# Kernel tuning notes

Measured on AMD Instinct MI355X. Metric: run time of the kernel, lower is better.

The kernel has to match this reference:

```python
import jax, jax.numpy as jnp
import numpy as np

B, S, D, H = 4, 2048, 1024, 16
DK = D // H

def setup_inputs() -> dict:
    key = jax.random.key(0)
    ks = jax.random.split(key, 8)
    scale = 1.0 / np.sqrt(D)
    return {
        'q': jax.random.normal(ks[0], (B, S, D), jnp.float32),
        'k': jax.random.normal(ks[1], (B, S, D), jnp.float32),
        'v': jax.random.normal(ks[2], (B, S, D), jnp.float32),
        'Wq': jax.random.normal(ks[3], (D, D), jnp.float32) * scale,
        'bq': jnp.zeros((D,), jnp.float32),
        'Wk': jax.random.normal(ks[4], (D, D), jnp.float32) * scale,
        'bk': jnp.zeros((D,), jnp.float32),
        'Wv': jax.random.normal(ks[5], (D, D), jnp.float32) * scale,
        'bv': jnp.zeros((D,), jnp.float32),
        'Wo': jax.random.normal(ks[6], (D, D), jnp.float32) * scale,
        'bo': jnp.zeros((D,), jnp.float32),
    }

def reference(q, k, v, Wq, bq, Wk, bk, Wv, bv, Wo, bo):
    # Linear projections (torch Linear: x @ W.T + b; here W stored as [in,out])
    qp = q @ Wq + bq  # [B,S,D]
    kp = k @ Wk + bk
    vp = v @ Wv + bv
    # split heads -> [B,H,S,DK]
    qh = qp.reshape(B, S, H, DK).transpose(0, 2, 1, 3)
    kh = kp.reshape(B, S, H, DK).transpose(0, 2, 1, 3)
    vh = vp.reshape(B, S, H, DK).transpose(0, 2, 1, 3)
    scores = jnp.einsum('bhqd,bhkd->bhqk', qh, kh) / jnp.sqrt(jnp.float32(DK))
    attn = jax.nn.softmax(scores, axis=-1)  # [B,H,S,S]
    out = jnp.einsum('bhqk,bhkd->bhqd', attn, vh)
    out = out.transpose(0, 2, 1, 3).reshape(B, S, D)
    return out @ Wo + bo
```

## Files before the change

### kernel.cpp

```cpp
#include <hip/hip_runtime.h>
#include <math.h>

#define SEQ 2048
#define DIM 1024
#define NH 16

typedef short s8v __attribute__((ext_vector_type(8)));
typedef float f4v __attribute__((ext_vector_type(4)));

__device__ __forceinline__ unsigned short f2bf(float x) {
    unsigned u = __float_as_uint(x);
    u += 0x7FFFu + ((u >> 16) & 1u);
    return (unsigned short)(u >> 16);
}
__device__ __forceinline__ unsigned short f2bf_fast(float x) {
    return (unsigned short)((__float_as_uint(x) + 0x8000u) >> 16);
}

__global__ void conv3_f32_bf16(const float* __restrict__ q, const float* __restrict__ k,
                               const float* __restrict__ v,
                               unsigned short* __restrict__ qb, unsigned short* __restrict__ kb,
                               unsigned short* __restrict__ vb, int n4) {
    const float* in = (blockIdx.y == 0) ? q : (blockIdx.y == 1) ? k : v;
    unsigned short* out = (blockIdx.y == 0) ? qb : (blockIdx.y == 1) ? kb : vb;
    int i = blockIdx.x * 256 + threadIdx.x;
    if (i >= n4) return;
    float4 x = ((const float4*)in)[i];
    ushort4 o;
    o.x = f2bf(x.x); o.y = f2bf(x.y); o.z = f2bf(x.z); o.w = f2bf(x.w);
    ((ushort4*)out)[i] = o;
}

__global__ __launch_bounds__(256)
void convT4_f32_bf16(const float* __restrict__ W0, const float* __restrict__ W1,
                     const float* __restrict__ W2, const float* __restrict__ W3,
                     unsigned short* __restrict__ T0, unsigned short* __restrict__ T1,
                     unsigned short* __restrict__ T2, unsigned short* __restrict__ T3) {
    const float* W = (blockIdx.z == 0) ? W0 : (blockIdx.z == 1) ? W1 : (blockIdx.z == 2) ? W2 : W3;
    unsigned short* WT = (blockIdx.z == 0) ? T0 : (blockIdx.z == 1) ? T1 : (blockIdx.z == 2) ? T2 : T3;
    __shared__ float T[64][65];
    const int t = threadIdx.x;
    const int n0 = blockIdx.x * 64, k0 = blockIdx.y * 64;
    #pragma unroll
    for (int i = 0; i < 4; i++) {
        int idx = t + i * 256;
        int r = idx >> 4, c4 = idx & 15;
        float4 v = *(const float4*)&W[(size_t)(k0 + r) * DIM + n0 + c4 * 4];
        T[r][c4 * 4 + 0] = v.x; T[r][c4 * 4 + 1] = v.y;
        T[r][c4 * 4 + 2] = v.z; T[r][c4 * 4 + 3] = v.w;
    }
    __syncthreads();
    #pragma unroll
    for (int i = 0; i < 4; i++) {
        int idx = t + i * 256;
        int rn = idx >> 4, c4 = idx & 15;
        ushort4 o;
        o.x = f2bf(T[c4 * 4 + 0][rn]);
        o.y = f2bf(T[c4 * 4 + 1][rn]);
        o.z = f2bf(T[c4 * 4 + 2][rn]);
        o.w = f2bf(T[c4 * 4 + 3][rn]);
        *(ushort4*)&WT[(size_t)(n0 + rn) * DIM + k0 + c4 * 4] = o;
    }
}

template<int MODE>
__device__ __forceinline__
void gemm_core(const unsigned short* __restrict__ A,
               const unsigned short* __restrict__ BT,
               const float* __restrict__ bias, void* __restrict__ outp,
               float scale, int bx, int by)
{
    __shared__ __align__(16) unsigned short As[128 * 64];
    __shared__ __align__(16) unsigned short Bs[128 * 64];
    const int t = threadIdx.x;
    const int lane = t & 63, w = t >> 6;
    const int l15 = lane & 15, quad = lane >> 4;
    const int bm = by * 128, bn = bx * 128;
    const int wm = (w & 1) * 64, wn = (w >> 1) * 64;
    const int lrow = lane >> 3, lcol = (lane & 7) * 8;

    f4v acc[4][4];
    #pragma unroll
    for (int mi = 0; mi < 4; mi++)
        #pragma unroll
        for (int ni = 0; ni < 4; ni++)
            acc[mi][ni] = (f4v){0.f, 0.f, 0.f, 0.f};

    for (int k0 = 0; k0 < DIM; k0 += 64) {
        __syncthreads();
        #pragma unroll
        for (int i = 0; i < 4; i++) {
            int ci = w + i * 4;
            int row = ci * 8 + lrow;
            __builtin_amdgcn_global_load_lds(
                (const __attribute__((address_space(1))) unsigned int*)
                    (A + (size_t)(bm + row) * DIM + k0 + lcol),
                (__attribute__((address_space(3))) unsigned int*)(As + ci * 8 * 64),
                16, 0, 0);
            __builtin_amdgcn_global_load_lds(
                (const __attribute__((address_space(1))) unsigned int*)
                    (BT + (size_t)(bn + row) * DIM + k0 + lcol),
                (__attribute__((address_space(3))) unsigned int*)(Bs + ci * 8 * 64),
                16, 0, 0);
        }
        __syncthreads();
        #pragma unroll
        for (int kc = 0; kc < 2; kc++) {
            const int ko = kc * 32 + quad * 8;
            s8v af[4], bf[4];
            #pragma unroll
            for (int mi = 0; mi < 4; mi++)
                af[mi] = *(const s8v*)&As[(wm + mi * 16 + l15) * 64 + ko];
            #pragma unroll
            for (int ni = 0; ni < 4; ni++)
                bf[ni] = *(const s8v*)&Bs[(wn + ni * 16 + l15) * 64 + ko];
            #pragma unroll
            for (int mi = 0; mi < 4; mi++)
                #pragma unroll
                for (int ni = 0; ni < 4; ni++)
                    acc[mi][ni] = __builtin_amdgcn_mfma_f32_16x16x32_bf16(
                        af[mi], bf[ni], acc[mi][ni], 0, 0, 0);
        }
    }

    #pragma unroll
    for (int mi = 0; mi < 4; mi++) {
        #pragma unroll
        for (int ni = 0; ni < 4; ni++) {
            #pragma unroll
            for (int r = 0; r < 4; r++) {
                int m = bm + wm + mi * 16 + quad * 4 + r;
                int n = bn + wn + ni * 16 + l15;
                float val = acc[mi][ni][r] + bias[n];
                if (MODE == 0) {
                    ((float*)outp)[(size_t)m * DIM + n] = val;
                } else {
                    val *= scale;
                    int b = m >> 11, s = m & (SEQ - 1);
                    int h = n >> 6, dk = n & 63;
                    ((unsigned short*)outp)[(((size_t)(b * NH + h)) * SEQ + s) * 64 + dk] = f2bf(val);
                }
            }
        }
    }
}

__global__ __launch_bounds__(256)
void qkv_gemm(const unsigned short* __restrict__ qb, const unsigned short* __restrict__ kb,
              const unsigned short* __restrict__ vb,
              const unsigned short* __restrict__ WqT, const unsigned short* __restrict__ WkT,
              const unsigned short* __restrict__ WvT,
              const float* __restrict__ bq, const float* __restrict__ bk,
              const float* __restrict__ bv,
              unsigned short* __restrict__ qp, unsigned short* __restrict__ kp,
              unsigned short* __restrict__ vp)
{
    const int z = blockIdx.z;
    const unsigned short* A  = (z == 0) ? qb : (z == 1) ? kb : vb;
    const unsigned short* BT = (z == 0) ? WqT : (z == 1) ? WkT : WvT;
    const float* bias        = (z == 0) ? bq : (z == 1) ? bk : bv;
    unsigned short* outp     = (z == 0) ? qp : (z == 1) ? kp : vp;
    float scale = (z == 0) ? 0.125f : 1.0f;
    gemm_core<1>(A, BT, bias, outp, scale, blockIdx.x, blockIdx.y);
}

__global__ __launch_bounds__(256)
void out_gemm(const unsigned short* __restrict__ A, const unsigned short* __restrict__ BT,
              const float* __restrict__ bias, float* __restrict__ outp)
{
    gemm_core<0>(A, BT, bias, outp, 1.0f, blockIdx.x, blockIdx.y);
}

__global__ __launch_bounds__(256)
void transp_v(const unsigned short* __restrict__ vp, unsigned short* __restrict__ vpT) {
    __shared__ unsigned short T[64 * 72];
    const int t = threadIdx.x;
    const int bh = blockIdx.y, s0 = blockIdx.x * 64;
    const int r = t >> 3, c = (t & 7) * 8;
    #pragma unroll
    for (int i = 0; i < 2; i++) {
        int row = r + i * 32;
        *(s8v*)&T[row * 72 + c] = *(const s8v*)&vp[((size_t)bh * SEQ + s0 + row) * 64 + c];
    }
    __syncthreads();
    #pragma unroll
    for (int i = 0; i < 2; i++) {
        int d = r + i * 32;
        s8v o;
        #pragma unroll
        for (int j = 0; j < 8; j++) o[j] = (short)T[(c + j) * 72 + d];
        *(s8v*)&vpT[((size_t)bh * 64 + d) * SEQ + s0 + c] = o;
    }
}

__global__ __launch_bounds__(256)
void attn_mfma(const unsigned short* __restrict__ Q,
               const unsigned short* __restrict__ Kp,
               const unsigned short* __restrict__ VT,
               unsigned short* __restrict__ AO)
{
    __shared__ __align__(16) unsigned short Ks[64 * 72];
    __shared__ __align__(16) unsigned short Vs[64 * 72];
    __shared__ __align__(16) unsigned short Ps[4][32 * 72];
    const int t = threadIdx.x;
    const int lane = t & 63, w = t >> 6;
    const int l15 = lane & 15, quad = lane >> 4;
    const int bh = blockIdx.y, q0 = blockIdx.x * 128;

    const unsigned short* qbase = Q + ((size_t)bh * SEQ + q0 + w * 32) * 64;
    const unsigned short* kbase = Kp + (size_t)bh * SEQ * 64;
    const unsigned short* vtbase = VT + (size_t)bh * 64 * SEQ;

    s8v qf[2][2];
    #pragma unroll
    for (int qs = 0; qs < 2; qs++)
        #pragma unroll
        for (int kc = 0; kc < 2; kc++)
            qf[qs][kc] = *(const s8v*)&qbase[(qs * 16 + l15) * 64 + kc * 32 + quad * 8];

    f4v o_acc[2][4];
    #pragma unroll
    for (int qs = 0; qs < 2; qs++)
        #pragma unroll
        for (int df = 0; df < 4; df++) o_acc[qs][df] = (f4v){0.f, 0.f, 0.f, 0.f};
    float l_part[2] = {0.f, 0.f};

    const int srow = t >> 3, scol = (t & 7) * 8;
    unsigned short* Pw = (unsigned short*)Ps[w];

    for (int kt = 0; kt < 32; kt++) {
        __syncthreads();
        #pragma unroll
        for (int i = 0; i < 2; i++) {
            int row = srow + i * 32;
            *(s8v*)&Ks[row * 72 + scol] =
                *(const s8v*)&kbase[((size_t)(kt * 64 + row)) * 64 + scol];
            *(s8v*)&Vs[row * 72 + scol] =
                *(const s8v*)&vtbase[(size_t)row * SEQ + kt * 64 + scol];
        }
        __syncthreads();

        f4v s_acc[2][4];
        #pragma unroll
        for (int qs = 0; qs < 2; qs++)
            #pragma unroll
            for (int mf = 0; mf < 4; mf++) s_acc[qs][mf] = (f4v){0.f, 0.f, 0.f, 0.f};
        #pragma unroll
        for (int kc = 0; kc < 2; kc++) {
            const int ko = kc * 32 + quad * 8;
            #pragma unroll
            for (int mf = 0; mf < 4; mf++) {
                s8v kf = *(const s8v*)&Ks[(mf * 16 + l15) * 72 + ko];
                #pragma unroll
                for (int qs = 0; qs < 2; qs++)
                    s_acc[qs][mf] = __builtin_amdgcn_mfma_f32_16x16x32_bf16(
                        kf, qf[qs][kc], s_acc[qs][mf], 0, 0, 0);
            }
        }

        #pragma unroll
        for (int qs = 0; qs < 2; qs++) {
            #pragma unroll
            for (int mf = 0; mf < 4; mf++) {
                float p0 = __expf(s_acc[qs][mf][0]);
                float p1 = __expf(s_acc[qs][mf][1]);
                float p2 = __expf(s_acc[qs][mf][2]);
                float p3 = __expf(s_acc[qs][mf][3]);
                l_part[qs] += (p0 + p1) + (p2 + p3);
                ushort4 pk;
                pk.x = f2bf_fast(p0); pk.y = f2bf_fast(p1);
                pk.z = f2bf_fast(p2); pk.w = f2bf_fast(p3);
                *(ushort4*)&Pw[(qs * 16 + l15) * 72 + mf * 16 + quad * 4] = pk;
            }
        }

        #pragma unroll
        for (int kc2 = 0; kc2 < 2; kc2++) {
            const int ko = kc2 * 32 + quad * 8;
            s8v pf0 = *(const s8v*)&Pw[(0 * 16 + l15) * 72 + ko];
            s8v pf1 = *(const s8v*)&Pw[(1 * 16 + l15) * 72 + ko];
            #pragma unroll
            for (int df = 0; df < 4; df++) {
                s8v vf = *(const s8v*)&Vs[(df * 16 + l15) * 72 + ko];
                o_acc[0][df] = __builtin_amdgcn_mfma_f32_16x16x32_bf16(pf0, vf, o_acc[0][df], 0, 0, 0);
                o_acc[1][df] = __builtin_amdgcn_mfma_f32_16x16x32_bf16(pf1, vf, o_acc[1][df], 0, 0, 0);
            }
        }
    }

    float lq[2][4];
    #pragma unroll
    for (int qs = 0; qs < 2; qs++) {
        float lt = l_part[qs];
        lt += __shfl_xor(lt, 16);
        lt += __shfl_xor(lt, 32);
        #pragma unroll
        for (int r = 0; r < 4; r++)
            lq[qs][r] = 1.0f / __shfl(lt, quad * 4 + r);
    }

    const int b = bh >> 4, h = bh & (NH - 1);
    #pragma unroll
    for (int qs = 0; qs < 2; qs++) {
        #pragma unroll
        for (int r = 0; r < 4; r++) {
            int s = q0 + w * 32 + qs * 16 + quad * 4 + r;
            #pragma unroll
            for (int df = 0; df < 4; df++)
                AO[((size_t)(b * SEQ + s)) * DIM + h * 64 + df * 16 + l15] =
                    f2bf(o_acc[qs][df][r] * lq[qs][r]);
        }
    }
}

extern "C" void kernel_launch(void* const* d_in, const int* in_sizes, int n_in,
                              void* d_out, int out_size, void* d_ws, size_t ws_size,
                              hipStream_t stream) {
    const float* q  = (const float*)d_in[0];
    const float* k  = (const float*)d_in[1];
    const float* v  = (const float*)d_in[2];
    const float* Wq = (const float*)d_in[3];
    const float* bq = (const float*)d_in[4];
    const float* Wk = (const float*)d_in[5];
    const float* bk = (const float*)d_in[6];
    const float* Wv = (const float*)d_in[7];
    const float* bv = (const float*)d_in[8];
    const float* Wo = (const float*)d_in[9];
    const float* bo = (const float*)d_in[10];
    float* out = (float*)d_out;

    const size_t MK = (size_t)4 * SEQ * DIM;
    const size_t WK = (size_t)DIM * DIM;
    unsigned short* wsu = (unsigned short*)d_ws;
    unsigned short* qb  = wsu;
    unsigned short* kb  = qb + MK;
    unsigned short* vb  = kb + MK;
    unsigned short* WqT = vb + MK;
    unsigned short* WkT = WqT + WK;
    unsigned short* WvT = WkT + WK;
    unsigned short* WoT = WvT + WK;
    unsigned short* qp  = WoT + WK;
    unsigned short* kp  = qp + MK;
    unsigned short* vp  = kp + MK;
    unsigned short* ao  = vp + MK;
    unsigned short* vpT = qb;

    const int n4 = (int)(MK / 4);
    conv3_f32_bf16<<<dim3((n4 + 255) / 256, 3), 256, 0, stream>>>(q, k, v, qb, kb, vb, n4);
    convT4_f32_bf16<<<dim3(16, 16, 4), 256, 0, stream>>>(Wq, Wk, Wv, Wo, WqT, WkT, WvT, WoT);

    qkv_gemm<<<dim3(DIM / 128, (4 * SEQ) / 128, 3), 256, 0, stream>>>(
        qb, kb, vb, WqT, WkT, WvT, bq, bk, bv, qp, kp, vp);

    transp_v<<<dim3(SEQ / 64, 4 * NH), 256, 0, stream>>>(vp, vpT);

    attn_mfma<<<dim3(SEQ / 128, 4 * NH), 256, 0, stream>>>(qp, kp, vpT, ao);

    out_gemm<<<dim3(DIM / 128, (4 * SEQ) / 128), 256, 0, stream>>>(ao, WoT, bo, out);
}
```

Before: 390.1 us.

## Load K/V MFMA fragments directly from global, use exp2 and packed bf16 convert

Removes the shared-memory staging of K and V tiles and their two block-wide barriers per iteration, so each wave loads its MFMA fragments straight from global memory (through cache). It also folds log2(e) into the Q scale so the softmax can use exp2f, and replaces manual bf16 rounding with the packed v_cvt_pk_bf16_f32 instruction. Without the staging, all four waves load the same K/V data separately, which puts more load on the L1/L2 caches and exposes global-load latency inside the MFMA loop in exchange for dropping the synchronisation.

Measured after the change: 654.9 us. 1.68x slower.

```diff
diff --git a/kernel.cpp b/kernel.cpp
--- a/kernel.cpp
+++ b/kernel.cpp
@@ -13,8 +13,10 @@
     u += 0x7FFFu + ((u >> 16) & 1u);
     return (unsigned short)(u >> 16);
 }
-__device__ __forceinline__ unsigned short f2bf_fast(float x) {
-    return (unsigned short)((__float_as_uint(x) + 0x8000u) >> 16);
+__device__ __forceinline__ unsigned cvt_pk_bf16(float lo, float hi) {
+    unsigned r;
+    asm("v_cvt_pk_bf16_f32 %0, %1, %2" : "=v"(r) : "v"(lo), "v"(hi));
+    return r;
 }
 
 __global__ void conv3_f32_bf16(const float* __restrict__ q, const float* __restrict__ k,
@@ -160,7 +162,7 @@
     const unsigned short* BT = (z == 0) ? WqT : (z == 1) ? WkT : WvT;
     const float* bias        = (z == 0) ? bq : (z == 1) ? bk : bv;
     unsigned short* outp     = (z == 0) ? qp : (z == 1) ? kp : vp;
-    float scale = (z == 0) ? 0.125f : 1.0f;
+    float scale = (z == 0) ? 0.18033688011112042f : 1.0f;
     gemm_core<1>(A, BT, bias, outp, scale, blockIdx.x, blockIdx.y);
 }
 
@@ -199,8 +201,6 @@
                const unsigned short* __restrict__ VT,
                unsigned short* __restrict__ AO)
 {
-    __shared__ __align__(16) unsigned short Ks[64 * 72];
-    __shared__ __align__(16) unsigned short Vs[64 * 72];
     __shared__ __align__(16) unsigned short Ps[4][32 * 72];
     const int t = threadIdx.x;
     const int lane = t & 63, w = t >> 6;
@@ -208,8 +208,8 @@
     const int bh = blockIdx.y, q0 = blockIdx.x * 128;
 
     const unsigned short* qbase = Q + ((size_t)bh * SEQ + q0 + w * 32) * 64;
-    const unsigned short* kbase = Kp + (size_t)bh * SEQ * 64;
-    const unsigned short* vtbase = VT + (size_t)bh * 64 * SEQ;
+    const unsigned short* kfb = Kp + (size_t)bh * SEQ * 64 + (size_t)l15 * 64 + quad * 8;
+    const unsigned short* vfb = VT + (size_t)bh * 64 * SEQ + (size_t)l15 * SEQ + quad * 8;
 
     s8v qf[2][2];
     #pragma unroll
@@ -225,21 +225,9 @@
         for (int df = 0; df < 4; df++) o_acc[qs][df] = (f4v){0.f, 0.f, 0.f, 0.f};
     float l_part[2] = {0.f, 0.f};
 
-    const int srow = t >> 3, scol = (t & 7) * 8;
     unsigned short* Pw = (unsigned short*)Ps[w];
 
     for (int kt = 0; kt < 32; kt++) {
-        __syncthreads();
-        #pragma unroll
-        for (int i = 0; i < 2; i++) {
-            int row = srow + i * 32;
-            *(s8v*)&Ks[row * 72 + scol] =
-                *(const s8v*)&kbase[((size_t)(kt * 64 + row)) * 64 + scol];
-            *(s8v*)&Vs[row * 72 + scol] =
-                *(const s8v*)&vtbase[(size_t)row * SEQ + kt * 64 + scol];
-        }
-        __syncthreads();
-
         f4v s_acc[2][4];
         #pragma unroll
         for (int qs = 0; qs < 2; qs++)
@@ -247,10 +235,9 @@
             for (int mf = 0; mf < 4; mf++) s_acc[qs][mf] = (f4v){0.f, 0.f, 0.f, 0.f};
         #pragma unroll
         for (int kc = 0; kc < 2; kc++) {
-            const int ko = kc * 32 + quad * 8;
             #pragma unroll
             for (int mf = 0; mf < 4; mf++) {
-                s8v kf = *(const s8v*)&Ks[(mf * 16 + l15) * 72 + ko];
+                s8v kf = *(const s8v*)&kfb[(size_t)(kt * 64 + mf * 16) * 64 + kc * 32];
                 #pragma unroll
                 for (int qs = 0; qs < 2; qs++)
                     s_acc[qs][mf] = __builtin_amdgcn_mfma_f32_16x16x32_bf16(
@@ -262,15 +249,15 @@
         for (int qs = 0; qs < 2; qs++) {
             #pragma unroll
             for (int mf = 0; mf < 4; mf++) {
-                float p0 = __expf(s_acc[qs][mf][0]);
-                float p1 = __expf(s_acc[qs][mf][1]);
-                float p2 = __expf(s_acc[qs][mf][2]);
-                float p3 = __expf(s_acc[qs][mf][3]);
+                float p0 = exp2f(s_acc[qs][mf][0]);
+                float p1 = exp2f(s_acc[qs][mf][1]);
+                float p2 = exp2f(s_acc[qs][mf][2]);
+                float p3 = exp2f(s_acc[qs][mf][3]);
                 l_part[qs] += (p0 + p1) + (p2 + p3);
-                ushort4 pk;
-                pk.x = f2bf_fast(p0); pk.y = f2bf_fast(p1);
-                pk.z = f2bf_fast(p2); pk.w = f2bf_fast(p3);
-                *(ushort4*)&Pw[(qs * 16 + l15) * 72 + mf * 16 + quad * 4] = pk;
+                uint2 pk;
+                pk.x = cvt_pk_bf16(p0, p1);
+                pk.y = cvt_pk_bf16(p2, p3);
+                *(uint2*)&Pw[(qs * 16 + l15) * 72 + mf * 16 + quad * 4] = pk;
             }
         }
 
@@ -281,7 +268,7 @@
             s8v pf1 = *(const s8v*)&Pw[(1 * 16 + l15) * 72 + ko];
             #pragma unroll
             for (int df = 0; df < 4; df++) {
-                s8v vf = *(const s8v*)&Vs[(df * 16 + l15) * 72 + ko];
+                s8v vf = *(const s8v*)&vfb[(size_t)(df * 16) * SEQ + kt * 64 + kc2 * 32];
                 o_acc[0][df] = __builtin_amdgcn_mfma_f32_16x16x32_bf16(pf0, vf, o_acc[0][df], 0, 0, 0);
                 o_acc[1][df] = __builtin_amdgcn_mfma_f32_16x16x32_bf16(pf1, vf, o_acc[1][df], 0, 0, 0);
             }
```
